# Optimization experiments

Measured on AMD Instinct MI355X. Metric: run time of the kernel, lower is better.

## Reference

```python
import jax, jax.numpy as jnp
import numpy as np

BS, K, FT = 256, 16, 512
HID = 256
EPS = 1e-5
SLOPE = 0.01  # LeakyReLU default negative slope


def setup_inputs() -> dict:
    key = jax.random.key(0)
    ks = jax.random.split(key, 6)
    cnn_output = jax.random.normal(ks[0], (BS, K, FT), dtype=jnp.float32)
    W1 = jax.random.normal(ks[1], (2 * FT, HID), dtype=jnp.float32) * (1.0 / np.sqrt(2 * FT))
    b1 = jnp.zeros((HID,), dtype=jnp.float32)
    gamma = jnp.ones((HID,), dtype=jnp.float32)
    beta = jnp.zeros((HID,), dtype=jnp.float32)
    W2 = jax.random.normal(ks[2], (HID, 1), dtype=jnp.float32) * (1.0 / np.sqrt(HID))
    b2 = jnp.zeros((1,), dtype=jnp.float32)
    return {"cnn_output": cnn_output, "W1": W1, "b1": b1, "gamma": gamma,
            "beta": beta, "W2": W2, "b2": b2}


def _aggregate_cat(cnn_output):
    bs, k, ft = cnn_output.shape
    iu, ju = jnp.triu_indices(k, k=1)          # pair order matches nested i<j loop
    p = iu.shape[0]
    shifts = (jnp.arange(p) % (bs - 1)) + 1    # 1,2,...,bs-1,1,2,...
    feat_i = jnp.transpose(cnn_output[:, iu], (1, 0, 2))  # [P, bs, ft]
    feat_j = jnp.transpose(cnn_output[:, ju], (1, 0, 2))  # [P, bs, ft]
    # roll(shift, dims=0)[b] == x[(b - shift) % bs]
    rows = (jnp.arange(bs)[None, :] - shifts[:, None]) % bs  # [P, bs]
    neg_j = cnn_output[rows, ju[:, None]]                    # [P, bs, ft]
    pos = jnp.concatenate([feat_i, feat_j], axis=-1).reshape(p * bs, 2 * ft)
    neg = jnp.concatenate([feat_i, neg_j], axis=-1).reshape(p * bs, 2 * ft)
    pairs = jnp.concatenate([pos, neg], axis=0)              # [2*P*bs, 2*ft]
    tgt = jnp.concatenate([jnp.ones((p * bs,), jnp.float32),
                           jnp.zeros((p * bs,), jnp.float32)])
    return pairs, tgt


def _relation_head(pairs, W1, b1, gamma, beta, W2, b2):
    h = pairs @ W1 + b1
    mean = jnp.mean(h, axis=0)
    var = jnp.var(h, axis=0)  # biased var, as torch BN in training mode
    hn = (h - mean) * jax.lax.rsqrt(var + EPS) * gamma + beta
    hn = jnp.where(hn >= 0, hn, SLOPE * hn)
    return (hn @ W2 + b2)[:, 0]


def _bce_with_logits(scores, tgt):
    # numerically stable BCEWithLogitsLoss (mean reduction)
    return jnp.mean(jnp.maximum(scores, 0.0) - scores * tgt
                    + jnp.log1p(jnp.exp(-jnp.abs(scores))))


def reference(cnn_output, W1, b1, gamma, beta, W2, b2):
    pairs, tgt = _aggregate_cat(cnn_output)
    scores = _relation_head(pairs, W1, b1, gamma, beta, W2, b2)
    loss = _bce_with_logits(scores, tgt)
    correct = jnp.stack([(scores > t / 10.0).astype(jnp.float32) == tgt
                         for t in range(1, 10)])  # [9, 2*P*bs] bool
    return loss, scores, correct
```

## Files before the change

### kernel.cpp

```cpp
#include <hip/hip_runtime.h>
#include <cmath>

#define KK 16
#define HID 256
#define NROWH 30720
#define NROW 61440
#define GM 4096
#define GK 512
#define GN 512
#define EPSV 1e-5f
#define SLOPEV 0.01f

#define BM 128
#define BN 64
#define BK 16
#define NT 32

__global__ __launch_bounds__(256) void k_gemm(const float* __restrict__ X,
                                              const float* __restrict__ W1,
                                              const float* __restrict__ b1,
                                              float* __restrict__ UV,
                                              float* __restrict__ zbuf) {
  if (blockIdx.x == 0) {
    for (int i = threadIdx.x; i < 5120; i += 256) zbuf[i] = 0.0f;
  }
  __shared__ float As[2][BK][BM];
  __shared__ float Bs[2][BK][BN];
  const int id = blockIdx.x;
  const int nt = id >> 5;
  const int mt = id & 31;
  const int m0 = mt * BM, n0 = nt * BN;
  const float* Wb = (n0 < HID) ? (W1 + n0) : (W1 + GK * HID + (n0 - HID));
  const int t = threadIdx.x;
  const int am  = t & 127;
  const int ak8 = (t >> 7) * 8;
  const int brr = t >> 4, bq = t & 15;
  const int ty = t >> 4, tx = t & 15;

  const float* Xp = X + (size_t)(m0 + am) * GK;

  float4 a40, a41, b4;
  float acc[8][4] = {};

  auto stage = [&](int it) {
    const int k0 = it * BK + ak8;
    a40 = *(const float4*)(Xp + k0);
    a41 = *(const float4*)(Xp + k0 + 4);
    b4  = *(const float4*)(Wb + (size_t)(it * BK + brr) * HID + bq * 4);
  };
  auto wr = [&](int buf) {
    As[buf][ak8 + 0][am] = a40.x;
    As[buf][ak8 + 1][am] = a40.y;
    As[buf][ak8 + 2][am] = a40.z;
    As[buf][ak8 + 3][am] = a40.w;
    As[buf][ak8 + 4][am] = a41.x;
    As[buf][ak8 + 5][am] = a41.y;
    As[buf][ak8 + 6][am] = a41.z;
    As[buf][ak8 + 7][am] = a41.w;
    *(float4*)&Bs[buf][brr][bq * 4] = b4;
  };

  stage(0);
  wr(0);
  __syncthreads();
  for (int it = 0; it < NT; ++it) {
    if (it + 1 < NT) stage(it + 1);
    const int buf = it & 1;
    #pragma unroll
    for (int kk = 0; kk < BK; ++kk) {
      float4 x0 = *(const float4*)&As[buf][kk][ty * 8];
      float4 x1 = *(const float4*)&As[buf][kk][ty * 8 + 4];
      float4 y  = *(const float4*)&Bs[buf][kk][tx * 4];
      float av[8] = {x0.x, x0.y, x0.z, x0.w, x1.x, x1.y, x1.z, x1.w};
      float bv[4] = {y.x, y.y, y.z, y.w};
      #pragma unroll
      for (int i = 0; i < 8; i++)
        #pragma unroll
        for (int j = 0; j < 4; j++)
          acc[i][j] = fmaf(av[i], bv[j], acc[i][j]);
    }
    if (it + 1 < NT) wr((it + 1) & 1);
    __syncthreads();
  }
  const int n = n0 + tx * 4;
  float4 add = {0.f, 0.f, 0.f, 0.f};
  if (n < HID) add = *(const float4*)&b1[n];
  #pragma unroll
  for (int i = 0; i < 8; i++) {
    const int m = m0 + ty * 8 + i;
    float4 v = {acc[i][0] + add.x, acc[i][1] + add.y, acc[i][2] + add.z, acc[i][3] + add.w};
    *(float4*)&UV[(size_t)m * GN + n] = v;
  }
}

__device__ __forceinline__ void decode_pair(int p, int& iu, int& ju) {
  int i = 0, q = p;
  while (q >= 15 - i) { q -= 15 - i; i++; }
  iu = i; ju = i + 1 + q;
}

__global__ __launch_bounds__(256) void k_stats(const float* __restrict__ UV,
                                               float* __restrict__ sums8) {
  const int bid = blockIdx.x;
  const int blk = (bid & 7) * 120 + (bid >> 3);
  const int p = blk >> 3;
  const int b0 = (blk & 7) * 32;
  const int f = threadIdx.x;
  int iu, ju; decode_pair(p, iu, ju);
  float s1 = 0.f, s2 = 0.f;
  for (int b = b0; b < b0 + 32; b++) {
    const int bi  = (b * KK + iu) * GN;
    const int bj1 = (b * KK + ju) * GN + HID;
    const int bj2 = (((b - p - 1) & 255) * KK + ju) * GN + HID;
    float u  = UV[bi + f];
    float h1 = u + UV[bj1 + f];
    float h2 = u + UV[bj2 + f];
    s1 += h1 + h2;
    s2 += h1 * h1 + h2 * h2;
  }
  float* dst = sums8 + (bid & 7) * 512;
  atomicAdd(dst + f, s1);
  atomicAdd(dst + 256 + f, s2);
}

__global__ __launch_bounds__(256) void k_finalize(const float* __restrict__ sums8,
                                                  const float* __restrict__ gamma,
                                                  const float* __restrict__ beta,
                                                  float* __restrict__ af,
                                                  float* __restrict__ cf) {
  const int f = threadIdx.x;
  float s1 = 0.f, s2 = 0.f;
  #pragma unroll
  for (int c = 0; c < 8; c++) {
    s1 += sums8[c * 512 + f];
    s2 += sums8[c * 512 + 256 + f];
  }
  float mean = s1 * (1.0f / NROW);
  float var  = s2 * (1.0f / NROW) - mean * mean;
  float a = gamma[f] * rsqrtf(var + EPSV);
  af[f] = a;
  cf[f] = beta[f] - mean * a;
}

__global__ __launch_bounds__(256) void k_scores(const float* __restrict__ UV,
                                                const float* __restrict__ af,
                                                const float* __restrict__ cf,
                                                const float* __restrict__ W2,
                                                const float* __restrict__ b2,
                                                float* __restrict__ out,
                                                float* __restrict__ lossAcc64) {
  const int bid = blockIdx.x;
  const int swz = (bid & 7) * 960 + (bid >> 3);
  const int wv0 = swz * 4;
  const int w = threadIdx.x >> 6;
  const int lane = threadIdx.x & 63;
  const int wv = wv0 + w;
  const int p = wv >> 8, b = wv & 255;
  int iu, ju; decode_pair(p, iu, ju);
  const int bi  = (b * KK + iu) * GN;
  const int bj1 = (b * KK + ju) * GN + HID;
  const int bj2 = (((b - p - 1) & 255) * KK + ju) * GN + HID;
  float sp = 0.f, sn = 0.f;
  #pragma unroll
  for (int r = 0; r < 4; r++) {
    int f = lane + r * 64;
    float u = UV[bi + f];
    float a = af[f], c = cf[f], ww = W2[f];
    float h1 = fmaf(a, u + UV[bj1 + f], c);
    h1 = h1 >= 0.f ? h1 : SLOPEV * h1;
    sp = fmaf(ww, h1, sp);
    float h2 = fmaf(a, u + UV[bj2 + f], c);
    h2 = h2 >= 0.f ? h2 : SLOPEV * h2;
    sn = fmaf(ww, h2, sn);
  }
  #pragma unroll
  for (int off = 32; off > 0; off >>= 1) {
    sp += __shfl_xor(sp, off, 64);
    sn += __shfl_xor(sn, off, 64);
  }
  __shared__ float sc[8];
  __shared__ float sbce[8];
  if (lane == 0) {
    float bb = b2[0];
    sc[w]     = sp + bb;
    sc[4 + w] = sn + bb;
  }
  __syncthreads();
  const int t = threadIdx.x;
  if (t < 8) {
    const int j = t & 3;
    const bool pos = t < 4;
    const int row = (pos ? 0 : NROWH) + wv0 + j;
    const float s = sc[t];
    out[1 + row] = s;
    float bce = fmaxf(s, 0.f) - (pos ? s : 0.f) + log1pf(expf(-fabsf(s)));
    sbce[t] = bce;
    #pragma unroll
    for (int tt = 1; tt <= 9; tt++) {
      bool pred = (double)s > (double)tt / 10.0;
      out[1 + NROW + (tt - 1) * NROW + row] = (pred == pos) ? 1.0f : 0.0f;
    }
  }
  __syncthreads();
  if (t == 0) {
    float bsum = sbce[0] + sbce[1] + sbce[2] + sbce[3]
               + sbce[4] + sbce[5] + sbce[6] + sbce[7];
    atomicAdd(&lossAcc64[(bid & 63) * 16], bsum);
  }
}

__global__ void k_loss(const float* __restrict__ lossAcc64, float* __restrict__ out) {
  const int t = threadIdx.x;
  float v = lossAcc64[t * 16];
  #pragma unroll
  for (int off = 32; off > 0; off >>= 1) v += __shfl_xor(v, off, 64);
  if (t == 0) out[0] = v * (1.0f / NROW);
}

extern "C" void kernel_launch(void* const* d_in, const int* in_sizes, int n_in,
                              void* d_out, int out_size, void* d_ws, size_t ws_size,
                              hipStream_t stream) {
  const float* X     = (const float*)d_in[0];
  const float* W1    = (const float*)d_in[1];
  const float* b1    = (const float*)d_in[2];
  const float* gamma = (const float*)d_in[3];
  const float* beta  = (const float*)d_in[4];
  const float* W2    = (const float*)d_in[5];
  const float* b2    = (const float*)d_in[6];
  float* out = (float*)d_out;

  float* UV        = (float*)d_ws;
  float* sums8     = UV + (size_t)GM * GN;
  float* lossAcc64 = sums8 + 8 * 512;
  float* af        = lossAcc64 + 1024;
  float* cf        = af + 256;

  hipLaunchKernelGGL(k_gemm,     dim3(256),  dim3(256), 0, stream, X, W1, b1, UV, sums8);
  hipLaunchKernelGGL(k_stats,    dim3(960),  dim3(256), 0, stream, UV, sums8);
  hipLaunchKernelGGL(k_finalize, dim3(1),    dim3(256), 0, stream, sums8, gamma, beta, af, cf);
  hipLaunchKernelGGL(k_scores,   dim3(7680), dim3(256), 0, stream, UV, af, cf, W2, b2, out, lossAcc64);
  hipLaunchKernelGGL(k_loss,     dim3(1),    dim3(64),  0, stream, lossAcc64, out);
}
```

Before: 131.9 us.

## Halve GEMM M-tile with XCD swizzle and fuse BN finalize into stats via ticket

The GEMM tile shrinks from 128 to 64 rows, doubling the grid to 512 blocks. Blocks are remapped so each XCD handles a contiguous band of M tiles, which should improve occupancy and L2 locality. The separate single-block finalize kernel is removed: the last k_stats block, detected with an atomic ticket counter plus a threadfence, computes the BN scale and shift. This saves one launch but adds an atomic and a fence to every stats block, and uses a float counter for the ticket.

```diff
diff --git a/kernel.cpp b/kernel.cpp
--- a/kernel.cpp
+++ b/kernel.cpp
@@ -11,10 +11,11 @@
 #define EPSV 1e-5f
 #define SLOPEV 0.01f
 
-#define BM 128
+#define BM 64
 #define BN 64
 #define BK 16
 #define NT 32
+#define NSTATB 960
 
 __global__ __launch_bounds__(256) void k_gemm(const float* __restrict__ X,
                                               const float* __restrict__ W1,
@@ -22,41 +23,35 @@
                                               float* __restrict__ UV,
                                               float* __restrict__ zbuf) {
   if (blockIdx.x == 0) {
-    for (int i = threadIdx.x; i < 5120; i += 256) zbuf[i] = 0.0f;
-  }
-  __shared__ float As[2][BK][BM];
+    for (int i = threadIdx.x; i < 5376; i += 256) zbuf[i] = 0.0f;
+  }
+  __shared__ float As[2][BK][68];
   __shared__ float Bs[2][BK][BN];
-  const int id = blockIdx.x;
-  const int nt = id >> 5;
-  const int mt = id & 31;
-  const int m0 = mt * BM, n0 = nt * BN;
+  const int id  = blockIdx.x;
+  const int xcd = id & 7, w8 = id >> 3;
+  const int mt  = xcd * 8 + (w8 >> 3);
+  const int nt  = w8 & 7;
+  const int m0  = mt * BM, n0 = nt * BN;
   const float* Wb = (n0 < HID) ? (W1 + n0) : (W1 + GK * HID + (n0 - HID));
   const int t = threadIdx.x;
-  const int am  = t & 127;
-  const int ak8 = (t >> 7) * 8;
+  const int am = t >> 2, aq = t & 3;
   const int brr = t >> 4, bq = t & 15;
   const int ty = t >> 4, tx = t & 15;
 
   const float* Xp = X + (size_t)(m0 + am) * GK;
 
-  float4 a40, a41, b4;
-  float acc[8][4] = {};
+  float4 a4, b4;
+  float acc[4][4] = {};
 
   auto stage = [&](int it) {
-    const int k0 = it * BK + ak8;
-    a40 = *(const float4*)(Xp + k0);
-    a41 = *(const float4*)(Xp + k0 + 4);
-    b4  = *(const float4*)(Wb + (size_t)(it * BK + brr) * HID + bq * 4);
+    a4 = *(const float4*)(Xp + it * BK + aq * 4);
+    b4 = *(const float4*)(Wb + (size_t)(it * BK + brr) * HID + bq * 4);
   };
   auto wr = [&](int buf) {
-    As[buf][ak8 + 0][am] = a40.x;
-    As[buf][ak8 + 1][am] = a40.y;
-    As[buf][ak8 + 2][am] = a40.z;
-    As[buf][ak8 + 3][am] = a40.w;
-    As[buf][ak8 + 4][am] = a41.x;
-    As[buf][ak8 + 5][am] = a41.y;
-    As[buf][ak8 + 6][am] = a41.z;
-    As[buf][ak8 + 7][am] = a41.w;
+    As[buf][aq * 4 + 0][am] = a4.x;
+    As[buf][aq * 4 + 1][am] = a4.y;
+    As[buf][aq * 4 + 2][am] = a4.z;
+    As[buf][aq * 4 + 3][am] = a4.w;
     *(float4*)&Bs[buf][brr][bq * 4] = b4;
   };
 
@@ -68,13 +63,12 @@
     const int buf = it & 1;
     #pragma unroll
     for (int kk = 0; kk < BK; ++kk) {
-      float4 x0 = *(const float4*)&As[buf][kk][ty * 8];
-      float4 x1 = *(const float4*)&As[buf][kk][ty * 8 + 4];
-      float4 y  = *(const float4*)&Bs[buf][kk][tx * 4];
-      float av[8] = {x0.x, x0.y, x0.z, x0.w, x1.x, x1.y, x1.z, x1.w};
+      float4 x = *(const float4*)&As[buf][kk][ty * 4];
+      float4 y = *(const float4*)&Bs[buf][kk][tx * 4];
+      float av[4] = {x.x, x.y, x.z, x.w};
       float bv[4] = {y.x, y.y, y.z, y.w};
       #pragma unroll
-      for (int i = 0; i < 8; i++)
+      for (int i = 0; i < 4; i++)
         #pragma unroll
         for (int j = 0; j < 4; j++)
           acc[i][j] = fmaf(av[i], bv[j], acc[i][j]);
@@ -86,8 +80,8 @@
   float4 add = {0.f, 0.f, 0.f, 0.f};
   if (n < HID) add = *(const float4*)&b1[n];
   #pragma unroll
-  for (int i = 0; i < 8; i++) {
-    const int m = m0 + ty * 8 + i;
+  for (int i = 0; i < 4; i++) {
+    const int m = m0 + ty * 4 + i;
     float4 v = {acc[i][0] + add.x, acc[i][1] + add.y, acc[i][2] + add.z, acc[i][3] + add.w};
     *(float4*)&UV[(size_t)m * GN + n] = v;
   }
@@ -100,7 +94,12 @@
 }
 
 __global__ __launch_bounds__(256) void k_stats(const float* __restrict__ UV,
-                                               float* __restrict__ sums8) {
+                                               float* __restrict__ sums8,
+                                               float* __restrict__ ticket,
+                                               const float* __restrict__ gamma,
+                                               const float* __restrict__ beta,
+                                               float* __restrict__ af,
+                                               float* __restrict__ cf) {
   const int bid = blockIdx.x;
   const int blk = (bid & 7) * 120 + (bid >> 3);
   const int p = blk >> 3;
@@ -121,25 +120,27 @@
   float* dst = sums8 + (bid & 7) * 512;
   atomicAdd(dst + f, s1);
   atomicAdd(dst + 256 + f, s2);
-}
-
-__global__ __launch_bounds__(256) void k_finalize(const float* __restrict__ sums8,
-                                                  const float* __restrict__ gamma,
-                                                  const float* __restrict__ beta,
-                                                  float* __restrict__ af,
-                                                  float* __restrict__ cf) {
-  const int f = threadIdx.x;
-  float s1 = 0.f, s2 = 0.f;
-  #pragma unroll
-  for (int c = 0; c < 8; c++) {
-    s1 += sums8[c * 512 + f];
-    s2 += sums8[c * 512 + 256 + f];
-  }
-  float mean = s1 * (1.0f / NROW);
-  float var  = s2 * (1.0f / NROW) - mean * mean;
-  float a = gamma[f] * rsqrtf(var + EPSV);
-  af[f] = a;
-  cf[f] = beta[f] - mean * a;
+  __shared__ int lastFlag;
+  __threadfence();
+  __syncthreads();
+  if (f == 0) {
+    float old = atomicAdd(ticket, 1.0f);
+    lastFlag = (old == (float)(NSTATB - 1)) ? 1 : 0;
+  }
+  __syncthreads();
+  if (lastFlag) {
+    float t1 = 0.f, t2 = 0.f;
+    #pragma unroll
+    for (int c = 0; c < 8; c++) {
+      t1 += sums8[c * 512 + f];
+      t2 += sums8[c * 512 + 256 + f];
+    }
+    float mean = t1 * (1.0f / NROW);
+    float var  = t2 * (1.0f / NROW) - mean * mean;
+    float a = gamma[f] * rsqrtf(var + EPSV);
+    af[f] = a;
+    cf[f] = beta[f] - mean * a;
+  }
 }
 
 __global__ __launch_bounds__(256) void k_scores(const float* __restrict__ UV,
@@ -231,13 +232,13 @@
 
   float* UV        = (float*)d_ws;
   float* sums8     = UV + (size_t)GM * GN;
-  float* lossAcc64 = sums8 + 8 * 512;
-  float* af        = lossAcc64 + 1024;
+  float* lossAcc64 = sums8 + 4096;
+  float* ticket    = lossAcc64 + 1024;
+  float* af        = ticket + 1;
   float* cf        = af + 256;
 
-  hipLaunchKernelGGL(k_gemm,     dim3(256),  dim3(256), 0, stream, X, W1, b1, UV, sums8);
-  hipLaunchKernelGGL(k_stats,    dim3(960),  dim3(256), 0, stream, UV, sums8);
-  hipLaunchKernelGGL(k_finalize, dim3(1),    dim3(256), 0, stream, sums8, gamma, beta, af, cf);
-  hipLaunchKernelGGL(k_scores,   dim3(7680), dim3(256), 0, stream, UV, af, cf, W2, b2, out, lossAcc64);
-  hipLaunchKernelGGL(k_loss,     dim3(1),    dim3(64),  0, stream, lossAcc64, out);
-}
+  hipLaunchKernelGGL(k_gemm,   dim3(512),  dim3(256), 0, stream, X, W1, b1, UV, sums8);
+  hipLaunchKernelGGL(k_stats,  dim3(NSTATB), dim3(256), 0, stream, UV, sums8, ticket, gamma, beta, af, cf);
+  hipLaunchKernelGGL(k_scores, dim3(7680), dim3(256), 0, stream, UV, af, cf, W2, b2, out, lossAcc64);
+  hipLaunchKernelGGL(k_loss,   dim3(1),    dim3(64),  0, stream, lossAcc64, out);
+}
```

After: 183.1 us. +38.8%, slower.
